# Performance work log

Measured on AMD Instinct MI355X. Metric: run time of the kernel, lower is better.

## Reference

```python
import jax, jax.numpy as jnp
import numpy as np

B, T, I, H = 256, 256, 2048, 128

def setup_inputs() -> dict:
    key = jax.random.key(0)
    ks = jax.random.split(key, 7)
    s = 1.0 / np.sqrt(H)  # torch RNN/Linear init scale
    return {
        "x": jax.random.normal(ks[0], (B, T, I), dtype=jnp.float32),
        "W_ih": jax.random.uniform(ks[1], (H, I), jnp.float32, -s, s),
        "W_hh": jax.random.uniform(ks[2], (H, H), jnp.float32, -s, s),
        "b_ih": jax.random.uniform(ks[3], (H,), jnp.float32, -s, s),
        "b_hh": jax.random.uniform(ks[4], (H,), jnp.float32, -s, s),
        "W_fc": jax.random.uniform(ks[5], (1, H), jnp.float32, -s, s),
        "b_fc": jax.random.uniform(ks[6], (1,), jnp.float32, -s, s),
    }

def reference(x, W_ih, W_hh, b_ih, b_hh, W_fc, b_fc):
    # Precompute input projection for all timesteps as one big GEMM: [B,T,H]
    xp = jnp.einsum('bti,hi->bth', x, W_ih) + (b_ih + b_hh)
    h0 = jnp.zeros((x.shape[0], W_hh.shape[0]), dtype=x.dtype)

    def step(h, xt):  # xt: [B,H]
        h = jnp.tanh(xt + h @ W_hh.T)
        return h, None

    hT, _ = jax.lax.scan(step, h0, jnp.swapaxes(xp, 0, 1))  # final hidden [B,H]
    out = hT @ W_fc.T + b_fc  # [B,1]
    return out.squeeze(1)     # [B]
```

## Files before the change

### kernel.cpp

```cpp
#include <hip/hip_runtime.h>
#include <hip/hip_bf16.h>
#include <math.h>

#define B_ 256
#define T_ 256
#define I_ 2048
#define H_ 128

#define BM 64
#define BK 64
#define NKT (I_ / BK)

typedef __attribute__((ext_vector_type(8))) short bf16x8;
typedef __attribute__((ext_vector_type(4))) float f32x4;
typedef _Float16 half2v __attribute__((ext_vector_type(2)));

static __device__ inline short f2bf(float f) {
    __hip_bfloat16 h = __float2bfloat16(f);
    return *reinterpret_cast<short*>(&h);
}

static __device__ inline bf16x8 pack8(float4 a, float4 b) {
    bf16x8 r;
    r[0] = f2bf(a.x); r[1] = f2bf(a.y); r[2] = f2bf(a.z); r[3] = f2bf(a.w);
    r[4] = f2bf(b.x); r[5] = f2bf(b.y); r[6] = f2bf(b.z); r[7] = f2bf(b.w);
    return r;
}

#define LGKM_BARRIER() do {                                  \
    asm volatile("s_waitcnt lgkmcnt(0)" ::: "memory");       \
    __builtin_amdgcn_sched_barrier(0);                       \
    __builtin_amdgcn_s_barrier();                            \
} while (0)

__global__ __launch_bounds__(256) void convW(
    const float* __restrict__ W, short* __restrict__ Wb)
{
    const int g = blockIdx.x * 256 + threadIdx.x;
    const float4 v0 = reinterpret_cast<const float4*>(W)[2 * g];
    const float4 v1 = reinterpret_cast<const float4*>(W)[2 * g + 1];
    reinterpret_cast<bf16x8*>(Wb)[g] = pack8(v0, v1);
}

__global__ __launch_bounds__(256, 4) void proj_mfma(
    const float* __restrict__ x, const short* __restrict__ Wb,
    const float* __restrict__ bih, const float* __restrict__ bhh,
    float* __restrict__ xp)
{
    __shared__ __align__(16) float As[2][BM * BK];

    const int tid  = threadIdx.x;
    const int lane = tid & 63;
    const int wid  = tid >> 6;
    const long row0 = (long)blockIdx.x * BM;

    const int fr = lane & 15;
    const int fq = lane >> 4;

    float biasr[2];
    #pragma unroll
    for (int n = 0; n < 2; ++n) {
        const int col = wid * 32 + n * 16 + fr;
        biasr[n] = bih[col] + bhh[col];
    }

    const int arow_l = lane >> 4;

    auto STAGE = [&](int tt, int buf) {
        const int kk = tt * BK;
        #pragma unroll
        for (int i = 0; i < 4; ++i) {
            const int r = (wid * 4 + i) * 4 + arow_l;
            const int u = (lane & 15) ^ (r & 15);
            const float* ga = x + (row0 + r) * I_ + kk + u * 4;
            __builtin_amdgcn_global_load_lds(
                (const __attribute__((address_space(1))) void*)ga,
                (__attribute__((address_space(3))) void*)&As[buf][(wid * 4 + i) * 256],
                16, 0, 0);
        }
    };

    auto LOADB = [&](int tt, bf16x8 bc[2][2]) {
        #pragma unroll
        for (int n = 0; n < 2; ++n) {
            const int R = wid * 32 + n * 16 + fr;
            #pragma unroll
            for (int kk = 0; kk < 2; ++kk)
                bc[n][kk] = *reinterpret_cast<const bf16x8*>(
                    Wb + (long)R * I_ + tt * BK + kk * 32 + fq * 8);
        }
    };

    f32x4 acc[4][2];
    #pragma unroll
    for (int m = 0; m < 4; ++m)
        #pragma unroll
        for (int n = 0; n < 2; ++n)
            acc[m][n] = (f32x4){0.f, 0.f, 0.f, 0.f};

    bf16x8 bcA[2][2], bcB[2][2];

    STAGE(0, 0);
    LOADB(0, bcA);
    __syncthreads();

    auto body = [&](int t, bf16x8 bcur[2][2], bf16x8 bnext[2][2], int p) {
        if (t + 1 < NKT) STAGE(t + 1, p ^ 1);
        #pragma unroll
        for (int kk = 0; kk < 2; ++kk) {
            #pragma unroll
            for (int m = 0; m < 4; ++m) {
                const int R  = m * 16 + fr;
                const int U0 = kk * 8 + fq * 2;
                const float4 a0 = *reinterpret_cast<const float4*>(
                    &As[p][R * 64 + ((U0 ^ (R & 15)) << 2)]);
                const float4 a1 = *reinterpret_cast<const float4*>(
                    &As[p][R * 64 + (((U0 + 1) ^ (R & 15)) << 2)]);
                const bf16x8 af = pack8(a0, a1);
                acc[m][0] = __builtin_amdgcn_mfma_f32_16x16x32_bf16(
                    af, bcur[0][kk], acc[m][0], 0, 0, 0);
                acc[m][1] = __builtin_amdgcn_mfma_f32_16x16x32_bf16(
                    af, bcur[1][kk], acc[m][1], 0, 0, 0);
            }
        }
        if (t + 1 < NKT) LOADB(t + 1, bnext);
        __syncthreads();
    };

    for (int t = 0; t < NKT; t += 2) {
        body(t,     bcA, bcB, 0);
        body(t + 1, bcB, bcA, 1);
    }

    #pragma unroll
    for (int n = 0; n < 2; ++n) {
        const int col = wid * 32 + n * 16 + fr;
        #pragma unroll
        for (int m = 0; m < 4; ++m) {
            const long rbase = row0 + m * 16 + fq * 4;
            #pragma unroll
            for (int j = 0; j < 4; ++j)
                xp[(rbase + j) * H_ + col] = acc[m][n][j] + biasr[n];
        }
    }
}

__global__ __launch_bounds__(256) void scan_kernel(
    const float* __restrict__ xp, const float* __restrict__ Whh,
    const float* __restrict__ Wfc, const float* __restrict__ bfc,
    float* __restrict__ out)
{
    __shared__ __align__(16) unsigned hpk[2][H_ / 2];

    const int tid  = threadIdx.x;
    const int lane = tid & 63;
    const int w    = tid >> 6;
    const int j    = w * 32 + (lane & 31);
    const int g    = lane >> 5;
    const int b    = blockIdx.x;

    half2v Wh[32];
    {
        const float4* wp = reinterpret_cast<const float4*>(&Whh[(long)j * H_ + g * 64]);
        #pragma unroll
        for (int q = 0; q < 16; ++q) {
            const float4 wv = wp[q];
            half2v p0, p1;
            p0[0] = (_Float16)wv.x; p0[1] = (_Float16)wv.y;
            p1[0] = (_Float16)wv.z; p1[1] = (_Float16)wv.w;
            Wh[2 * q]     = p0;
            Wh[2 * q + 1] = p1;
        }
    }
    if (tid < H_ / 2) hpk[0][tid] = 0u;

    const float* xprow = xp + (long)b * T_ * H_ + j;
    float xa = xprow[0 * H_];
    float xb = xprow[1 * H_];
    float xc = xprow[2 * H_];
    float xd = xprow[3 * H_];
    __syncthreads();

    auto body = [&](int t, float xpv) {
        const uint4* hp = reinterpret_cast<const uint4*>(&hpk[t & 1][g * 32]);
        float a0 = 0.f, a1 = 0.f, a2 = 0.f, a3 = 0.f;
        #pragma unroll
        for (int q = 0; q < 8; ++q) {
            const uint4 u = hp[q];
            a0 = __builtin_amdgcn_fdot2(__builtin_bit_cast(half2v, u.x), Wh[4*q+0], a0, false);
            a1 = __builtin_amdgcn_fdot2(__builtin_bit_cast(half2v, u.y), Wh[4*q+1], a1, false);
            a2 = __builtin_amdgcn_fdot2(__builtin_bit_cast(half2v, u.z), Wh[4*q+2], a2, false);
            a3 = __builtin_amdgcn_fdot2(__builtin_bit_cast(half2v, u.w), Wh[4*q+3], a3, false);
        }
        float part = (a0 + a1) + (a2 + a3);
        part += __shfl_xor(part, 32);
        const float pre = part + xpv;
        const float e = __expf(2.f * pre);
        const float h = 1.f - 2.f / (e + 1.f);
        if (g == 0) {
            reinterpret_cast<unsigned short*>(&hpk[(t + 1) & 1][0])[j] =
                __builtin_bit_cast(unsigned short, (_Float16)h);
        }
        LGKM_BARRIER();
    };

    for (int t = 0; t < T_; t += 4) {
        float xu;
        xu = xa; if (t + 4 < T_) xa = xprow[(long)(t + 4) * H_];
        body(t + 0, xu);
        xu = xb; if (t + 5 < T_) xb = xprow[(long)(t + 5) * H_];
        body(t + 1, xu);
        xu = xc; if (t + 6 < T_) xc = xprow[(long)(t + 6) * H_];
        body(t + 2, xu);
        xu = xd; if (t + 7 < T_) xd = xprow[(long)(t + 7) * H_];
        body(t + 3, xu);
    }

    if (w == 0) {
        const unsigned u = hpk[0][lane];
        const half2v hh = __builtin_bit_cast(half2v, u);
        float v = (float)hh[0] * Wfc[2 * lane] + (float)hh[1] * Wfc[2 * lane + 1];
        #pragma unroll
        for (int off = 32; off > 0; off >>= 1) v += __shfl_down(v, off);
        if (lane == 0) out[b] = v + bfc[0];
    }
}

extern "C" void kernel_launch(void* const* d_in, const int* in_sizes, int n_in,
                              void* d_out, int out_size, void* d_ws, size_t ws_size,
                              hipStream_t stream)
{
    const float* x   = (const float*)d_in[0];
    const float* Wih = (const float*)d_in[1];
    const float* Whh = (const float*)d_in[2];
    const float* bih = (const float*)d_in[3];
    const float* bhh = (const float*)d_in[4];
    const float* Wfc = (const float*)d_in[5];
    const float* bfc = (const float*)d_in[6];
    float* out = (float*)d_out;
    float* xp  = (float*)d_ws;
    short* Wb  = (short*)((char*)d_ws + (size_t)B_ * T_ * H_ * sizeof(float));

    convW<<<dim3((H_ * I_) / (256 * 8)), dim3(256), 0, stream>>>(Wih, Wb);
    proj_mfma<<<dim3((B_ * T_) / BM), dim3(256), 0, stream>>>(x, Wb, bih, bhh, xp);
    scan_kernel<<<dim3(B_), dim3(256), 0, stream>>>(xp, Whh, Wfc, bfc, out);
}
```

Before: 231.0 us.

## Drop LDS staging in projection GEMM; load A fragments directly from global

The projection kernel no longer stages x tiles into shared memory with global_load_lds and barriers. Each wave now owns a 32x64 output sub-tile and loads its A fragments straight from global memory into registers, double-buffered in two register banks. B fragments are read from global per k-step. This removes LDS traffic and per-tile __syncthreads, but each x row is now loaded by two waves (n halves), so global/L2 traffic rises and loads become less coalesced.

```diff
diff --git a/kernel.cpp b/kernel.cpp
--- a/kernel.cpp
+++ b/kernel.cpp
@@ -8,8 +8,7 @@
 #define H_ 128
 
 #define BM 64
-#define BK 64
-#define NKT (I_ / BK)
+#define NKS 64
 
 typedef __attribute__((ext_vector_type(8))) short bf16x8;
 typedef __attribute__((ext_vector_type(4))) float f32x4;
@@ -47,100 +46,73 @@
     const float* __restrict__ bih, const float* __restrict__ bhh,
     float* __restrict__ xp)
 {
-    __shared__ __align__(16) float As[2][BM * BK];
-
     const int tid  = threadIdx.x;
     const int lane = tid & 63;
     const int wid  = tid >> 6;
-    const long row0 = (long)blockIdx.x * BM;
+    const int mh   = wid & 1;
+    const int nh   = wid >> 1;
+    const long row0 = (long)blockIdx.x * BM + mh * 32;
+    const int  col0 = nh * 64;
 
     const int fr = lane & 15;
     const int fq = lane >> 4;
 
-    float biasr[2];
+    const float* ax0 = x + (row0 + fr) * I_ + fq * 8;
+    const float* ax1 = x + (row0 + 16 + fr) * I_ + fq * 8;
+    const short* bw  = Wb + (long)(col0 + fr) * I_ + fq * 8;
+
+    float biasr[4];
     #pragma unroll
-    for (int n = 0; n < 2; ++n) {
-        const int col = wid * 32 + n * 16 + fr;
+    for (int n = 0; n < 4; ++n) {
+        const int col = col0 + n * 16 + fr;
         biasr[n] = bih[col] + bhh[col];
     }
 
-    const int arow_l = lane >> 4;
-
-    auto STAGE = [&](int tt, int buf) {
-        const int kk = tt * BK;
-        #pragma unroll
-        for (int i = 0; i < 4; ++i) {
-            const int r = (wid * 4 + i) * 4 + arow_l;
-            const int u = (lane & 15) ^ (r & 15);
-            const float* ga = x + (row0 + r) * I_ + kk + u * 4;
-            __builtin_amdgcn_global_load_lds(
-                (const __attribute__((address_space(1))) void*)ga,
-                (__attribute__((address_space(3))) void*)&As[buf][(wid * 4 + i) * 256],
-                16, 0, 0);
-        }
+    f32x4 acc[2][4];
+    #pragma unroll
+    for (int m = 0; m < 2; ++m)
+        #pragma unroll
+        for (int n = 0; n < 4; ++n)
+            acc[m][n] = (f32x4){0.f, 0.f, 0.f, 0.f};
+
+    float4 Aa[4], Ab[4];
+
+    auto LOADA = [&](int k, float4* bank) {
+        bank[0] = *reinterpret_cast<const float4*>(ax0 + k);
+        bank[1] = *reinterpret_cast<const float4*>(ax0 + k + 4);
+        bank[2] = *reinterpret_cast<const float4*>(ax1 + k);
+        bank[3] = *reinterpret_cast<const float4*>(ax1 + k + 4);
     };
 
-    auto LOADB = [&](int tt, bf16x8 bc[2][2]) {
-        #pragma unroll
-        for (int n = 0; n < 2; ++n) {
-            const int R = wid * 32 + n * 16 + fr;
-            #pragma unroll
-            for (int kk = 0; kk < 2; ++kk)
-                bc[n][kk] = *reinterpret_cast<const bf16x8*>(
-                    Wb + (long)R * I_ + tt * BK + kk * 32 + fq * 8);
+    auto COMPUTE = [&](int t, float4* bank) {
+        const bf16x8 a0 = pack8(bank[0], bank[1]);
+        const bf16x8 a1 = pack8(bank[2], bank[3]);
+        const short* bk = bw + t * 32;
+        #pragma unroll
+        for (int n = 0; n < 4; ++n) {
+            const bf16x8 bf = *reinterpret_cast<const bf16x8*>(bk + (long)n * 16 * I_);
+            acc[0][n] = __builtin_amdgcn_mfma_f32_16x16x32_bf16(a0, bf, acc[0][n], 0, 0, 0);
+            acc[1][n] = __builtin_amdgcn_mfma_f32_16x16x32_bf16(a1, bf, acc[1][n], 0, 0, 0);
         }
     };
 
-    f32x4 acc[4][2];
+    LOADA(0, Aa);
+    for (int t = 0; t < NKS; t += 2) {
+        if (t + 1 < NKS) LOADA((t + 1) * 32, Ab);
+        COMPUTE(t, Aa);
+        if (t + 2 < NKS) LOADA((t + 2) * 32, Aa);
+        COMPUTE(t + 1, Ab);
+    }
+
     #pragma unroll
-    for (int m = 0; m < 4; ++m)
-        #pragma unroll
-        for (int n = 0; n < 2; ++n)
-            acc[m][n] = (f32x4){0.f, 0.f, 0.f, 0.f};
-
-    bf16x8 bcA[2][2], bcB[2][2];
-
-    STAGE(0, 0);
-    LOADB(0, bcA);
-    __syncthreads();
-
-    auto body = [&](int t, bf16x8 bcur[2][2], bf16x8 bnext[2][2], int p) {
-        if (t + 1 < NKT) STAGE(t + 1, p ^ 1);
-        #pragma unroll
-        for (int kk = 0; kk < 2; ++kk) {
-            #pragma unroll
-            for (int m = 0; m < 4; ++m) {
-                const int R  = m * 16 + fr;
-                const int U0 = kk * 8 + fq * 2;
-                const float4 a0 = *reinterpret_cast<const float4*>(
-                    &As[p][R * 64 + ((U0 ^ (R & 15)) << 2)]);
-                const float4 a1 = *reinterpret_cast<const float4*>(
-                    &As[p][R * 64 + (((U0 + 1) ^ (R & 15)) << 2)]);
-                const bf16x8 af = pack8(a0, a1);
-                acc[m][0] = __builtin_amdgcn_mfma_f32_16x16x32_bf16(
-                    af, bcur[0][kk], acc[m][0], 0, 0, 0);
-                acc[m][1] = __builtin_amdgcn_mfma_f32_16x16x32_bf16(
-                    af, bcur[1][kk], acc[m][1], 0, 0, 0);
-            }
-        }
-        if (t + 1 < NKT) LOADB(t + 1, bnext);
-        __syncthreads();
-    };
-
-    for (int t = 0; t < NKT; t += 2) {
-        body(t,     bcA, bcB, 0);
-        body(t + 1, bcB, bcA, 1);
-    }
-
-    #pragma unroll
-    for (int n = 0; n < 2; ++n) {
-        const int col = wid * 32 + n * 16 + fr;
-        #pragma unroll
-        for (int m = 0; m < 4; ++m) {
+    for (int n = 0; n < 4; ++n) {
+        const int col = col0 + n * 16 + fr;
+        #pragma unroll
+        for (int m = 0; m < 2; ++m) {
             const long rbase = row0 + m * 16 + fq * 4;
             #pragma unroll
-            for (int j = 0; j < 4; ++j)
-                xp[(rbase + j) * H_ + col] = acc[m][n][j] + biasr[n];
+            for (int i = 0; i < 4; ++i)
+                xp[(rbase + i) * H_ + col] = acc[m][n][i] + biasr[n];
         }
     }
 }
```

Result: slower. 345.3 us (+49.5%).
